# Kernel optimization log

Hardware: AMD Instinct MI355X
Metric: run time of the kernel (lower is better)

The kernel has to match this reference:

```python
import jax, jax.numpy as jnp
import numpy as np

B, T, C, H = 4, 2048, 1024, 128  # batch, block_size, n_embds, head_size


def setup_inputs() -> dict:
    key = jax.random.key(0)
    k1, k2, k3, k4 = jax.random.split(key, 4)
    x = jax.random.normal(k1, (B, T, C), dtype=jnp.float32)
    # Linear(n_embds, head_size, bias=False) weights, stored as [C, H] so q = x @ Wq
    s = C ** -0.5
    Wq = jax.random.normal(k2, (C, H), dtype=jnp.float32) * s
    Wk = jax.random.normal(k3, (C, H), dtype=jnp.float32) * s
    Wv = jax.random.normal(k4, (C, H), dtype=jnp.float32) * s
    return {"x": x, "Wq": Wq, "Wk": Wk, "Wv": Wv}


def reference(x, Wq, Wk, Wv):
    # q, k, v projections (no bias)
    q = x @ Wq  # [B, T, H]
    k = x @ Wk  # [B, T, H]
    v = x @ Wv  # [B, T, H]
    scale = q.shape[-1] ** -0.5
    wei = jnp.einsum('btd,bsd->bts', q, k) * scale  # [B, T, T]
    # causal mask: positions where tril == 0 (upper triangle) get -inf
    t = wei.shape[1]
    causal = jnp.tril(jnp.ones((t, t), dtype=bool))
    wei = jnp.where(causal, wei, -jnp.inf)
    # NOTE: source uses F.softmax(wei, dim=1) -> normalize over the QUERY axis
    wei = jax.nn.softmax(wei, axis=1)
    out = wei @ v  # [B, T, H]
    return out
```

## Files before the change

### kernel.cpp

```cpp
#include <hip/hip_runtime.h>
#include <math.h>

#define B_ 4
#define T_ 2048
#define C_ 1024
#define H_ 128
#define RCHUNK 128
#define NCHUNK (T_ / RCHUNK)
#define NSCH 32

typedef unsigned short u16;
typedef unsigned int   u32;
typedef short short8  __attribute__((ext_vector_type(8)));
typedef short short4v __attribute__((ext_vector_type(4)));
typedef float floatx4 __attribute__((ext_vector_type(4)));

__device__ __forceinline__ u16 f2bf(float f) {
    union { float f; u32 u; } v; v.f = f;
    return (u16)((v.u + 0x7fffu + ((v.u >> 16) & 1u)) >> 16);
}
__device__ __forceinline__ float bf2f(u16 h) {
    union { u32 u; float f; } v; v.u = ((u32)h) << 16;
    return v.f;
}

__global__ __launch_bounds__(256) void convert_w_kernel(
    const float* __restrict__ Wq, const float* __restrict__ Wk,
    const float* __restrict__ Wv, u16* __restrict__ Wt)
{
    const int k0 = blockIdx.x * 64, n0 = blockIdx.y * 64, widx = blockIdx.z;
    const float* W = (widx == 0) ? Wq : (widx == 1) ? Wk : Wv;

    __shared__ float ts[64][68];
    for (int i = threadIdx.x; i < 64 * 16; i += 256) {
        int r = i >> 4, c4 = i & 15;
        float4 v = *(const float4*)&W[(size_t)(k0 + r) * H_ + n0 + c4 * 4];
        ts[r][c4 * 4 + 0] = v.x; ts[r][c4 * 4 + 1] = v.y;
        ts[r][c4 * 4 + 2] = v.z; ts[r][c4 * 4 + 3] = v.w;
    }
    __syncthreads();
    for (int i = threadIdx.x; i < 64 * 16; i += 256) {
        int n = i >> 4, k4 = i & 15;
        short4v o;
        #pragma unroll
        for (int j = 0; j < 4; ++j) o[j] = (short)f2bf(ts[k4 * 4 + j][n]);
        *(short4v*)&Wt[(size_t)widx * H_ * C_ + (size_t)(n0 + n) * C_ + k0 + k4 * 4] = o;
    }
}

__global__ __launch_bounds__(256) void qkv_gemm_kernel(
    const float* __restrict__ x, const u16* __restrict__ Wt,
    u16* __restrict__ Qb, u16* __restrict__ Kb, u16* __restrict__ Vt)
{
    const int m0   = blockIdx.x * 64;
    const int widx = blockIdx.y;
    const u16* Wg = Wt + (size_t)widx * H_ * C_;

    __shared__ u16 As[64 * 136];
    __shared__ u16 Bs[128 * 136];

    const int w    = threadIdx.x >> 6;
    const int lane = threadIdx.x & 63;
    const int q    = lane >> 4, r = lane & 15;

    floatx4 acc[8] = {};

    for (int k0 = 0; k0 < C_; k0 += 128) {
        for (int i = threadIdx.x; i < 64 * 16; i += 256) {
            int rr = i >> 4, c = i & 15;
            const float* xg = &x[(size_t)(m0 + rr) * C_ + k0 + c * 8];
            float4 a = *(const float4*)xg;
            float4 b = *(const float4*)(xg + 4);
            short8 o;
            o[0]=(short)f2bf(a.x); o[1]=(short)f2bf(a.y);
            o[2]=(short)f2bf(a.z); o[3]=(short)f2bf(a.w);
            o[4]=(short)f2bf(b.x); o[5]=(short)f2bf(b.y);
            o[6]=(short)f2bf(b.z); o[7]=(short)f2bf(b.w);
            *(short8*)&As[rr * 136 + c * 8] = o;
        }
        for (int i = threadIdx.x; i < 128 * 16; i += 256) {
            int rr = i >> 4, c = i & 15;
            *(float4*)&Bs[rr * 136 + c * 8] =
                *(const float4*)&Wg[(size_t)rr * C_ + k0 + c * 8];
        }
        __syncthreads();

        #pragma unroll
        for (int kk = 0; kk < 4; ++kk) {
            short8 af = *(const short8*)&As[(16 * w + r) * 136 + kk * 32 + q * 8];
            #pragma unroll
            for (int nt = 0; nt < 8; ++nt) {
                short8 bf = *(const short8*)&Bs[(16 * nt + r) * 136 + kk * 32 + q * 8];
                acc[nt] = __builtin_amdgcn_mfma_f32_16x16x32_bf16(af, bf, acc[nt], 0, 0, 0);
            }
        }
        __syncthreads();
    }

    if (widx == 2) {
        const int bb  = m0 / T_;
        const int tt0 = (m0 - bb * T_) + 16 * w + q * 4;
        #pragma unroll
        for (int nt = 0; nt < 8; ++nt) {
            short4v o;
            #pragma unroll
            for (int reg = 0; reg < 4; ++reg) o[reg] = (short)f2bf(acc[nt][reg]);
            *(short4v*)&Vt[((size_t)bb * H_ + 16 * nt + r) * T_ + tt0] = o;
        }
    } else {
        u16* dst = (widx == 0) ? Qb : Kb;
        #pragma unroll
        for (int nt = 0; nt < 8; ++nt)
            #pragma unroll
            for (int reg = 0; reg < 4; ++reg) {
                int mm = m0 + 16 * w + q * 4 + reg;
                int nn = 16 * nt + r;
                dst[(size_t)mm * H_ + nn] = f2bf(acc[nt][reg]);
            }
    }
}

__global__ __launch_bounds__(256) void scores_kernel(
    const u16* __restrict__ Qb, const u16* __restrict__ Kb,
    u16* __restrict__ S, float* __restrict__ pm, float* __restrict__ pl)
{
    const int si = blockIdx.x;
    const int ti = blockIdx.y;
    const int b  = blockIdx.z;
    if (si > ti) return;
    const int t0 = ti * 128, s0 = si * 128;
    const bool diag = (si == ti);

    __shared__ u16 smem[2 * 128 * 136];
    u16* Qs = smem;
    u16* Ks = smem + 128 * 136;

    const u16* Qg = Qb + ((size_t)b * T_ + t0) * H_;
    const u16* Kg = Kb + ((size_t)b * T_ + s0) * H_;

    for (int i = threadIdx.x; i < 128 * 16; i += 256) {
        int rr = i >> 4, c = i & 15;
        *(float4*)&Qs[rr * 136 + c * 8] = *(const float4*)&Qg[(size_t)rr * H_ + c * 8];
        *(float4*)&Ks[rr * 136 + c * 8] = *(const float4*)&Kg[(size_t)rr * H_ + c * 8];
    }
    __syncthreads();

    const int w    = threadIdx.x >> 6;
    const int lane = threadIdx.x & 63;
    const int q    = lane >> 4, r = lane & 15;

    floatx4 acc[2][8] = {};
    #pragma unroll
    for (int kk = 0; kk < 4; ++kk) {
        short8 a0 = *(const short8*)&Qs[(32 * w +      r) * 136 + kk * 32 + q * 8];
        short8 a1 = *(const short8*)&Qs[(32 * w + 16 + r) * 136 + kk * 32 + q * 8];
        #pragma unroll
        for (int nt = 0; nt < 8; ++nt) {
            short8 bf = *(const short8*)&Ks[(16 * nt + r) * 136 + kk * 32 + q * 8];
            acc[0][nt] = __builtin_amdgcn_mfma_f32_16x16x32_bf16(a0, bf, acc[0][nt], 0, 0, 0);
            acc[1][nt] = __builtin_amdgcn_mfma_f32_16x16x32_bf16(a1, bf, acc[1][nt], 0, 0, 0);
        }
    }
    __syncthreads();

    u16*   tile = smem;
    float* redm = (float*)(smem + 128 * 136);
    float* redl = redm + 16 * 128;

    const float scale = 0.08838834764831845f;
    #pragma unroll
    for (int nt = 0; nt < 8; ++nt) {
        const int sl = 16 * nt + r;
        float v[8];  bool val[8];
        #pragma unroll
        for (int mt = 0; mt < 2; ++mt)
            #pragma unroll
            for (int reg = 0; reg < 4; ++reg) {
                const int j  = mt * 4 + reg;
                const int tl = 32 * w + 16 * mt + q * 4 + reg;
                v[j] = acc[mt][nt][reg] * scale;
                tile[tl * 136 + sl] = f2bf(v[j]);
                val[j] = (!diag) || (tl >= sl);
            }
        float mx = -INFINITY;
        #pragma unroll
        for (int j = 0; j < 8; ++j) mx = fmaxf(mx, val[j] ? v[j] : -INFINITY);
        float sm = 0.f;
        #pragma unroll
        for (int j = 0; j < 8; ++j) if (val[j]) sm += __expf(v[j] - mx);
        redm[(4 * w + q) * 128 + sl] = mx;
        redl[(4 * w + q) * 128 + sl] = sm;
    }
    __syncthreads();

    if (threadIdx.x < 128) {
        const int c = threadIdx.x;
        float M = -INFINITY;
        #pragma unroll
        for (int g = 0; g < 16; ++g) M = fmaxf(M, redm[g * 128 + c]);
        float L = 0.f;
        #pragma unroll
        for (int g = 0; g < 16; ++g) {
            float lg = redl[g * 128 + c];
            if (lg > 0.f) L += lg * __expf(redm[g * 128 + c] - M);
        }
        const size_t o = ((size_t)b * NCHUNK + ti) * T_ + s0 + c;
        pm[o] = M;
        pl[o] = L;
    }

    for (int i = threadIdx.x; i < 128 * 16; i += 256) {
        int tl = i >> 4, cc = (i >> 3) & 1, c8 = i & 7;
        u16* Sg = S + (((size_t)b * NSCH + 2 * si + cc) * T_ + t0 + tl) * 64;
        *(float4*)&Sg[c8 * 8] = *(float4*)&tile[tl * 136 + cc * 64 + c8 * 8];
    }
}

__global__ __launch_bounds__(256) void stats_reduce_kernel(
    const float* __restrict__ pm, const float* __restrict__ pl,
    float* __restrict__ m, float* __restrict__ linv)
{
    const int idx = blockIdx.x * 256 + threadIdx.x;
    const int b = idx >> 11, s = idx & (T_ - 1);
    const int c0 = s >> 7;

    float M = -INFINITY;
    for (int c = c0; c < NCHUNK; ++c)
        M = fmaxf(M, pm[((size_t)b * NCHUNK + c) * T_ + s]);

    float L = 0.f;
    for (int c = c0; c < NCHUNK; ++c) {
        float mc = pm[((size_t)b * NCHUNK + c) * T_ + s];
        float lc = pl[((size_t)b * NCHUNK + c) * T_ + s];
        if (lc > 0.f) L += lc * __expf(mc - M);
    }
    m[idx]    = M;
    linv[idx] = 1.0f / L;
}

#define RST 132
__global__ __launch_bounds__(512) void out_kernel(
    const u16* __restrict__ S, const u16* __restrict__ Vt,
    const float* __restrict__ m, const float* __restrict__ linv,
    float* __restrict__ out)
{
    const int b  = blockIdx.y;
    const int tb = (int)(gridDim.x - 1 - blockIdx.x);
    const int t0 = tb * 16;
    const int nchunks = (t0 + 79) >> 6;

    const int w    = threadIdx.x >> 6;
    const int lane = threadIdx.x & 63;
    const int q    = lane >> 4, r = lane & 15;
    const int t    = t0 + r;

    const u16*   SB  = S    + (size_t)b * NSCH * T_ * 64;
    const float* mB  = m    + (size_t)b * T_;
    const float* lB  = linv + (size_t)b * T_;
    const u16*   VtB = Vt   + (size_t)b * H_ * T_;

    floatx4 acc[8] = {};

    short8 sc[2];  float4 mc[2][2], lc[2][2];

    int ci = w;
    if (ci < nchunks) {
        const u16* Sc = SB + ((size_t)ci * T_ + t) * 64;
        const int  s0 = ci * 64;
        #pragma unroll
        for (int kk = 0; kk < 2; ++kk) {
            const int sl = kk * 32 + q * 8;
            sc[kk]    = *(const short8*)&Sc[sl];
            mc[kk][0] = *(const float4*)&mB[s0 + sl];
            mc[kk][1] = *(const float4*)&mB[s0 + sl + 4];
            lc[kk][0] = *(const float4*)&lB[s0 + sl];
            lc[kk][1] = *(const float4*)&lB[s0 + sl + 4];
        }
    }

    while (ci < nchunks) {
        const int s0 = ci * 64;
        const int cn = ci + 8;

        short8 sn[2];  float4 mn[2][2], ln[2][2];
        if (cn < nchunks) {
            const u16* Sc = SB + ((size_t)cn * T_ + t) * 64;
            const int  s0n = cn * 64;
            #pragma unroll
            for (int kk = 0; kk < 2; ++kk) {
                const int sl = kk * 32 + q * 8;
                sn[kk]    = *(const short8*)&Sc[sl];
                mn[kk][0] = *(const float4*)&mB[s0n + sl];
                mn[kk][1] = *(const float4*)&mB[s0n + sl + 4];
                ln[kk][0] = *(const float4*)&lB[s0n + sl];
                ln[kk][1] = *(const float4*)&lB[s0n + sl + 4];
            }
        }

        #pragma unroll
        for (int kk = 0; kk < 2; ++kk) {
            const int sb = s0 + kk * 32 + q * 8;
            float mv[8], lv[8];
            *(float4*)&mv[0] = mc[kk][0];  *(float4*)&mv[4] = mc[kk][1];
            *(float4*)&lv[0] = lc[kk][0];  *(float4*)&lv[4] = lc[kk][1];

            short8 af;
            #pragma unroll
            for (int j = 0; j < 8; ++j) {
                float wj = 0.f;
                if (sb + j <= t)
                    wj = __expf(bf2f((u16)sc[kk][j]) - mv[j]) * lv[j];
                af[j] = (short)f2bf(wj);
            }
            #pragma unroll
            for (int nt = 0; nt < 8; ++nt) {
                short8 bf = *(const short8*)&VtB[(size_t)(16 * nt + r) * T_ + sb];
                acc[nt] = __builtin_amdgcn_mfma_f32_16x16x32_bf16(af, bf, acc[nt], 0, 0, 0);
            }
        }

        #pragma unroll
        for (int kk = 0; kk < 2; ++kk) {
            sc[kk] = sn[kk];
            mc[kk][0] = mn[kk][0];  mc[kk][1] = mn[kk][1];
            lc[kk][0] = ln[kk][0];  lc[kk][1] = ln[kk][1];
        }
        ci = cn;
    }

    __shared__ float red[8][16 * RST];
    #pragma unroll
    for (int nt = 0; nt < 8; ++nt)
        #pragma unroll
        for (int reg = 0; reg < 4; ++reg)
            red[w][(q * 4 + reg) * RST + 16 * nt + r] = acc[nt][reg];
    __syncthreads();

    float* outB = out + ((size_t)b * T_ + t0) * H_;
    for (int i = threadIdx.x; i < 16 * 128; i += 512) {
        const int row = i >> 7, col = i & 127;
        float sum = 0.f;
        #pragma unroll
        for (int g = 0; g < 8; ++g) sum += red[g][row * RST + col];
        outB[i] = sum;
    }
}

extern "C" void kernel_launch(void* const* d_in, const int* in_sizes, int n_in,
                              void* d_out, int out_size, void* d_ws, size_t ws_size,
                              hipStream_t stream) {
    const float* x  = (const float*)d_in[0];
    const float* Wq = (const float*)d_in[1];
    const float* Wk = (const float*)d_in[2];
    const float* Wv = (const float*)d_in[3];
    float* out = (float*)d_out;

    u16*   S    = (u16*)d_ws;
    float* m    = (float*)(S + (size_t)B_ * T_ * T_);
    float* linv = m + (size_t)B_ * T_;
    u16*   Wt   = (u16*)(linv + (size_t)B_ * T_);
    u16*   Qb   = Wt + (size_t)3 * H_ * C_;
    u16*   Kb   = Qb + (size_t)B_ * T_ * H_;
    u16*   Vt   = Kb + (size_t)B_ * T_ * H_;

    float* pm = (float*)d_out;
    float* pl = pm + (size_t)B_ * NCHUNK * T_;

    convert_w_kernel  <<<dim3(C_ / 64, H_ / 64, 3),    dim3(256), 0, stream>>>(Wq, Wk, Wv, Wt);
    qkv_gemm_kernel   <<<dim3(B_ * T_ / 64, 3),        dim3(256), 0, stream>>>(x, Wt, Qb, Kb, Vt);
    scores_kernel     <<<dim3(16, 16, B_),             dim3(256), 0, stream>>>(Qb, Kb, S, pm, pl);
    stats_reduce_kernel<<<dim3(B_ * T_ / 256),         dim3(256), 0, stream>>>(pm, pl, m, linv);
    out_kernel        <<<dim3(T_ / 16, B_),            dim3(512), 0, stream>>>(S, Vt, m, linv, out);
}
```

Baseline: 171.4 us.

## Store chunk-local exponentials in scores and fold stats reduction into out kernel

The scores kernel now computes the per-chunk column max first, then stores exp(s - M_chunk) in bf16 instead of raw scaled scores, and writes chunk-local max and sum. The separate stats_reduce kernel is removed. Each out_kernel block instead recomputes the global column max and sum for the columns it needs and builds a per-column factor in shared memory, so the inner loop becomes a single multiply per element rather than an exp with a causal check. This saves one launch and the per-element exp work in the hot loop, at the cost of redundant stats reduction across out blocks, an extra sync and pass in the scores kernel, and 8 KB more shared memory per out block.

```diff
diff --git a/kernel.cpp b/kernel.cpp
--- a/kernel.cpp
+++ b/kernel.cpp
@@ -1,4 +1,5 @@
 #include <hip/hip_runtime.h>
+#include <hip/hip_bf16.h>
 #include <math.h>
 
 #define B_ 4
@@ -16,8 +17,8 @@
 typedef float floatx4 __attribute__((ext_vector_type(4)));
 
 __device__ __forceinline__ u16 f2bf(float f) {
-    union { float f; u32 u; } v; v.f = f;
-    return (u16)((v.u + 0x7fffu + ((v.u >> 16) & 1u)) >> 16);
+    __hip_bfloat16 h = __float2bfloat16(f);
+    union { __hip_bfloat16 h; u16 u; } v; v.h = h; return v.u;
 }
 __device__ __forceinline__ float bf2f(u16 h) {
     union { u32 u; float f; } v; v.u = ((u32)h) << 16;
@@ -166,30 +167,23 @@
     u16*   tile = smem;
     float* redm = (float*)(smem + 128 * 136);
     float* redl = redm + 16 * 128;
+    float* Mrow = redl + 16 * 128;
 
     const float scale = 0.08838834764831845f;
+
     #pragma unroll
     for (int nt = 0; nt < 8; ++nt) {
         const int sl = 16 * nt + r;
-        float v[8];  bool val[8];
+        float mx = -INFINITY;
         #pragma unroll
         for (int mt = 0; mt < 2; ++mt)
             #pragma unroll
             for (int reg = 0; reg < 4; ++reg) {
-                const int j  = mt * 4 + reg;
                 const int tl = 32 * w + 16 * mt + q * 4 + reg;
-                v[j] = acc[mt][nt][reg] * scale;
-                tile[tl * 136 + sl] = f2bf(v[j]);
-                val[j] = (!diag) || (tl >= sl);
-            }
-        float mx = -INFINITY;
-        #pragma unroll
-        for (int j = 0; j < 8; ++j) mx = fmaxf(mx, val[j] ? v[j] : -INFINITY);
-        float sm = 0.f;
-        #pragma unroll
-        for (int j = 0; j < 8; ++j) if (val[j]) sm += __expf(v[j] - mx);
+                const bool vl = (!diag) || (tl >= sl);
+                mx = fmaxf(mx, vl ? acc[mt][nt][reg] : -INFINITY);
+            }
         redm[(4 * w + q) * 128 + sl] = mx;
-        redl[(4 * w + q) * 128 + sl] = sm;
     }
     __syncthreads();
 
@@ -198,15 +192,37 @@
         float M = -INFINITY;
         #pragma unroll
         for (int g = 0; g < 16; ++g) M = fmaxf(M, redm[g * 128 + c]);
+        M *= scale;
+        Mrow[c] = M;
+        pm[((size_t)b * NCHUNK + ti) * T_ + s0 + c] = M;
+    }
+    __syncthreads();
+
+    #pragma unroll
+    for (int nt = 0; nt < 8; ++nt) {
+        const int sl = 16 * nt + r;
+        const float M = Mrow[sl];
+        float sm = 0.f;
+        #pragma unroll
+        for (int mt = 0; mt < 2; ++mt)
+            #pragma unroll
+            for (int reg = 0; reg < 4; ++reg) {
+                const int tl = 32 * w + 16 * mt + q * 4 + reg;
+                const bool vl = (!diag) || (tl >= sl);
+                const float e = vl ? __expf(acc[mt][nt][reg] * scale - M) : 0.f;
+                sm += e;
+                tile[tl * 136 + sl] = f2bf(e);
+            }
+        redl[(4 * w + q) * 128 + sl] = sm;
+    }
+    __syncthreads();
+
+    if (threadIdx.x < 128) {
+        const int c = threadIdx.x;
         float L = 0.f;
         #pragma unroll
-        for (int g = 0; g < 16; ++g) {
-            float lg = redl[g * 128 + c];
-            if (lg > 0.f) L += lg * __expf(redm[g * 128 + c] - M);
-        }
-        const size_t o = ((size_t)b * NCHUNK + ti) * T_ + s0 + c;
-        pm[o] = M;
-        pl[o] = L;
+        for (int g = 0; g < 16; ++g) L += redl[g * 128 + c];
+        pl[((size_t)b * NCHUNK + ti) * T_ + s0 + c] = L;
     }
 
     for (int i = threadIdx.x; i < 128 * 16; i += 256) {
@@ -216,37 +232,16 @@
     }
 }
 
-__global__ __launch_bounds__(256) void stats_reduce_kernel(
-    const float* __restrict__ pm, const float* __restrict__ pl,
-    float* __restrict__ m, float* __restrict__ linv)
-{
-    const int idx = blockIdx.x * 256 + threadIdx.x;
-    const int b = idx >> 11, s = idx & (T_ - 1);
-    const int c0 = s >> 7;
-
-    float M = -INFINITY;
-    for (int c = c0; c < NCHUNK; ++c)
-        M = fmaxf(M, pm[((size_t)b * NCHUNK + c) * T_ + s]);
-
-    float L = 0.f;
-    for (int c = c0; c < NCHUNK; ++c) {
-        float mc = pm[((size_t)b * NCHUNK + c) * T_ + s];
-        float lc = pl[((size_t)b * NCHUNK + c) * T_ + s];
-        if (lc > 0.f) L += lc * __expf(mc - M);
-    }
-    m[idx]    = M;
-    linv[idx] = 1.0f / L;
-}
-
 #define RST 132
 __global__ __launch_bounds__(512) void out_kernel(
     const u16* __restrict__ S, const u16* __restrict__ Vt,
-    const float* __restrict__ m, const float* __restrict__ linv,
+    const float* __restrict__ pm, const float* __restrict__ pl,
     float* __restrict__ out)
 {
     const int b  = blockIdx.y;
     const int tb = (int)(gridDim.x - 1 - blockIdx.x);
     const int t0 = tb * 16;
+    const int ti = t0 >> 7;
     const int nchunks = (t0 + 79) >> 6;
 
     const int w    = threadIdx.x >> 6;
@@ -254,64 +249,62 @@
     const int q    = lane >> 4, r = lane & 15;
     const int t    = t0 + r;
 
-    const u16*   SB  = S    + (size_t)b * NSCH * T_ * 64;
-    const float* mB  = m    + (size_t)b * T_;
-    const float* lB  = linv + (size_t)b * T_;
-    const u16*   VtB = Vt   + (size_t)b * H_ * T_;
+    const u16* SB  = S  + (size_t)b * NSCH * T_ * 64;
+    const u16* VtB = Vt + (size_t)b * H_ * T_;
+
+    __shared__ float fs[T_];
+    __shared__ float red[8][16 * RST];
 
     floatx4 acc[8] = {};
-
-    short8 sc[2];  float4 mc[2][2], lc[2][2];
+    short8 sc[2];
 
     int ci = w;
     if (ci < nchunks) {
         const u16* Sc = SB + ((size_t)ci * T_ + t) * 64;
-        const int  s0 = ci * 64;
-        #pragma unroll
-        for (int kk = 0; kk < 2; ++kk) {
-            const int sl = kk * 32 + q * 8;
-            sc[kk]    = *(const short8*)&Sc[sl];
-            mc[kk][0] = *(const float4*)&mB[s0 + sl];
-            mc[kk][1] = *(const float4*)&mB[s0 + sl + 4];
-            lc[kk][0] = *(const float4*)&lB[s0 + sl];
-            lc[kk][1] = *(const float4*)&lB[s0 + sl + 4];
-        }
-    }
+        sc[0] = *(const short8*)&Sc[q * 8];
+        sc[1] = *(const short8*)&Sc[32 + q * 8];
+    }
+
+    const int smax = 64 * nchunks;
+    const float* pmB = pm + (size_t)b * NCHUNK * T_;
+    const float* plB = pl + (size_t)b * NCHUNK * T_;
+    for (int s = threadIdx.x; s < smax; s += 512) {
+        const int c0 = s >> 7;
+        float M = -INFINITY;
+        for (int c = c0; c < NCHUNK; ++c)
+            M = fmaxf(M, pmB[(size_t)c * T_ + s]);
+        float L = 0.f;
+        for (int c = c0; c < NCHUNK; ++c) {
+            const float lg = plB[(size_t)c * T_ + s];
+            if (lg > 0.f) L += lg * __expf(pmB[(size_t)c * T_ + s] - M);
+        }
+        fs[s] = (ti >= c0) ? __expf(pmB[(size_t)ti * T_ + s] - M) / L : 0.f;
+    }
+    __syncthreads();
 
     while (ci < nchunks) {
         const int s0 = ci * 64;
         const int cn = ci + 8;
 
-        short8 sn[2];  float4 mn[2][2], ln[2][2];
+        short8 sn[2];
         if (cn < nchunks) {
             const u16* Sc = SB + ((size_t)cn * T_ + t) * 64;
-            const int  s0n = cn * 64;
-            #pragma unroll
-            for (int kk = 0; kk < 2; ++kk) {
-                const int sl = kk * 32 + q * 8;
-                sn[kk]    = *(const short8*)&Sc[sl];
-                mn[kk][0] = *(const float4*)&mB[s0n + sl];
-                mn[kk][1] = *(const float4*)&mB[s0n + sl + 4];
-                ln[kk][0] = *(const float4*)&lB[s0n + sl];
-                ln[kk][1] = *(const float4*)&lB[s0n + sl + 4];
-            }
+            sn[0] = *(const short8*)&Sc[q * 8];
+            sn[1] = *(const short8*)&Sc[32 + q * 8];
         }
 
         #pragma unroll
         for (int kk = 0; kk < 2; ++kk) {
             const int sb = s0 + kk * 32 + q * 8;
-            float mv[8], lv[8];
-            *(float4*)&mv[0] = mc[kk][0];  *(float4*)&mv[4] = mc[kk][1];
-            *(float4*)&lv[0] = lc[kk][0];  *(float4*)&lv[4] = lc[kk][1];
+            float fv[8];
+            *(float4*)&fv[0] = *(const float4*)&fs[sb];
+            *(float4*)&fv[4] = *(const float4*)&fs[sb + 4];
 
             short8 af;
             #pragma unroll
-            for (int j = 0; j < 8; ++j) {
-                float wj = 0.f;
-                if (sb + j <= t)
-                    wj = __expf(bf2f((u16)sc[kk][j]) - mv[j]) * lv[j];
-                af[j] = (short)f2bf(wj);
-            }
+            for (int j = 0; j < 8; ++j)
+                af[j] = (short)f2bf(bf2f((u16)sc[kk][j]) * fv[j]);
+
             #pragma unroll
             for (int nt = 0; nt < 8; ++nt) {
                 short8 bf = *(const short8*)&VtB[(size_t)(16 * nt + r) * T_ + sb];
@@ -319,16 +312,11 @@
             }
         }
 
-        #pragma unroll
-        for (int kk = 0; kk < 2; ++kk) {
-            sc[kk] = sn[kk];
-            mc[kk][0] = mn[kk][0];  mc[kk][1] = mn[kk][1];
-            lc[kk][0] = ln[kk][0];  lc[kk][1] = ln[kk][1];
-        }
+        sc[0] = sn[0];
+        sc[1] = sn[1];
         ci = cn;
     }
 
-    __shared__ float red[8][16 * RST];
     #pragma unroll
     for (int nt = 0; nt < 8; ++nt)
         #pragma unroll
@@ -355,20 +343,16 @@
     const float* Wv = (const float*)d_in[3];
     float* out = (float*)d_out;
 
-    u16*   S    = (u16*)d_ws;
-    float* m    = (float*)(S + (size_t)B_ * T_ * T_);
-    float* linv = m + (size_t)B_ * T_;
-    u16*   Wt   = (u16*)(linv + (size_t)B_ * T_);
+    u16*   Sb   = (u16*)d_ws;
+    u16*   Wt   = Sb + (size_t)B_ * T_ * T_;
     u16*   Qb   = Wt + (size_t)3 * H_ * C_;
     u16*   Kb   = Qb + (size_t)B_ * T_ * H_;
     u16*   Vt   = Kb + (size_t)B_ * T_ * H_;
-
-    float* pm = (float*)d_out;
-    float* pl = pm + (size_t)B_ * NCHUNK * T_;
-
-    convert_w_kernel  <<<dim3(C_ / 64, H_ / 64, 3),    dim3(256), 0, stream>>>(Wq, Wk, Wv, Wt);
-    qkv_gemm_kernel   <<<dim3(B_ * T_ / 64, 3),        dim3(256), 0, stream>>>(x, Wt, Qb, Kb, Vt);
-    scores_kernel     <<<dim3(16, 16, B_),             dim3(256), 0, stream>>>(Qb, Kb, S, pm, pl);
-    stats_reduce_kernel<<<dim3(B_ * T_ / 256),         dim3(256), 0, stream>>>(pm, pl, m, linv);
-    out_kernel        <<<dim3(T_ / 16, B_),            dim3(512), 0, stream>>>(S, Vt, m, linv, out);
-}
+    float* pm   = (float*)(Vt + (size_t)B_ * T_ * H_);
+    float* pl   = pm + (size_t)B_ * NCHUNK * T_;
+
+    convert_w_kernel <<<dim3(C_ / 64, H_ / 64, 3), dim3(256), 0, stream>>>(Wq, Wk, Wv, Wt);
+    qkv_gemm_kernel  <<<dim3(B_ * T_ / 64, 3),     dim3(256), 0, stream>>>(x, Wt, Qb, Kb, Vt);
+    scores_kernel    <<<dim3(16, 16, B_),          dim3(256), 0, stream>>>(Qb, Kb, Sb, pm, pl);
+    out_kernel       <<<dim3(T_ / 16, B_),         dim3(512), 0, stream>>>(Sb, Vt, pm, pl, out);
+}
```

New measurement: 185.0 us. +7.9%, slower.
